# Optimization experiments

Hardware: AMD Instinct MI355X
Metric: run time of the kernel (lower is better)

Reference implementation:

```python
import jax, jax.numpy as jnp
import numpy as np

CUTOFF = 5.0

def ssp(x):
    # shifted softplus: ln(0.5*e^x + 0.5)
    return jax.nn.softplus(x) - jnp.log(2.0).astype(x.dtype)

def cosine_cutoff(r):
    return 0.5 * (jnp.cos(jnp.pi * r / CUTOFF) + 1.0) * (r < CUTOFF).astype(r.dtype)

def setup_inputs() -> dict:
    key = jax.random.key(0)
    ks = jax.random.split(key, 16)
    B, A, N, Nd, F, Din, Dout, Th = 2, 512, 1024, 64, 64, 128, 128, 25
    inp = {}
    inp['x'] = jax.random.normal(ks[0], (B, A, Din), dtype=jnp.float32)
    inp['r_double'] = jax.random.uniform(ks[1], (B, A, Nd), dtype=jnp.float32)
    inp['r_ij'] = jax.random.uniform(ks[2], (B, A, N), dtype=jnp.float32)
    inp['r_ik'] = jax.random.uniform(ks[3], (B, A, N), dtype=jnp.float32)
    inp['r_jk'] = jax.random.uniform(ks[4], (B, A, N), dtype=jnp.float32)
    inp['neighbors'] = jax.random.randint(ks[5], (B, A, Nd), 0, A, dtype=jnp.int32)
    inp['neighbor_mask'] = jnp.ones((B, A, Nd), dtype=jnp.float32)
    inp['neighbors_j'] = jax.random.randint(ks[6], (B, A, N), 0, A, dtype=jnp.int32)
    inp['neighbors_k'] = jax.random.randint(ks[7], (B, A, N), 0, A, dtype=jnp.int32)
    inp['triple_masks'] = jnp.ones((B, A, N), dtype=jnp.float32)
    inp['d_ijk'] = jax.random.uniform(ks[8], (B, A, N, Th), dtype=jnp.float32)
    s = 0.1
    inp['W_in2f'] = s * jax.random.normal(ks[9], (Din, F), dtype=jnp.float32)
    inp['W_t1'] = s * jax.random.normal(ks[10], (Th, F), dtype=jnp.float32)
    inp['b_t1'] = jnp.zeros((F,), dtype=jnp.float32)
    inp['W_t2'] = s * jax.random.normal(ks[11], (F, F), dtype=jnp.float32)
    inp['b_t2'] = jnp.zeros((F,), dtype=jnp.float32)
    inp['W_f2out'] = s * jax.random.normal(ks[12], (F, Dout), dtype=jnp.float32)
    inp['b_f2out'] = jnp.zeros((Dout,), dtype=jnp.float32)
    return inp

def reference(x, r_double, r_ij, r_ik, r_jk, neighbors, neighbor_mask,
              neighbors_j, neighbors_k, triple_masks, d_ijk,
              W_in2f, W_t1, b_t1, W_t2, b_t2, W_f2out, b_f2out):
    # Triple filter: 2-layer MLP on angular basis, modulated by cutoffs
    h = ssp(jnp.einsum('bant,tf->banf', d_ijk, W_t1) + b_t1)
    W_triple = jnp.einsum('banf,fg->bang', h, W_t2) + b_t2
    W_triple = W_triple * cosine_cutoff(r_ij)[..., None] * cosine_cutoff(r_ik)[..., None]

    # in2f: (B, A, F)
    y = jnp.einsum('bad,df->baf', x, W_in2f)
    B, A, N = neighbors_j.shape
    F = y.shape[-1]
    # gather neighbor features along atom axis
    yj = jnp.take_along_axis(y, neighbors_j.reshape(B, A * N, 1), axis=1).reshape(B, A, N, F)
    yk = jnp.take_along_axis(y, neighbors_k.reshape(B, A * N, 1), axis=1).reshape(B, A, N, F)
    w_ij = r_ij[..., None]
    w_ik = r_ik[..., None]
    y = (w_ij * yj + w_ik * yk) / (w_ij + w_ik)
    # filter multiply + masked sum aggregation over triples axis
    y = y * W_triple
    y = jnp.sum(y * triple_masks[..., None], axis=2)
    # f2out with shifted-softplus activation
    out = ssp(jnp.einsum('baf,fo->bao', y, W_f2out) + b_f2out)
    return out
```

## Files before the change

kernel.cpp:

```cpp
#include <hip/hip_runtime.h>
#include <hip/hip_fp16.h>

#define BB 2
#define AA 512
#define NN 1024
#define FF 64
#define DIN 128
#define DOUT 128
#define TH 25
#define ASTRIDE 40
#define HSTRIDE 72
#define NSPLIT 4

typedef _Float16 half8 __attribute__((ext_vector_type(8)));
typedef float floatx4 __attribute__((ext_vector_type(4)));

__device__ __forceinline__ float ssp_f(float x) {
    return __logf(0.5f * __expf(x) + 0.5f);
}

__device__ __forceinline__ float cutcos(float r) {
    float c = 0.5f * (__cosf(r * (3.14159265358979323846f / 5.0f)) + 1.0f);
    return (r < 5.0f) ? c : 0.0f;
}

__device__ __forceinline__ __half2 ssp2(__half2 x) {
    const __half2 hlf = __float2half2_rn(0.5f);
    return h2log(__hfma2(h2exp(x), hlf, hlf));
}

__device__ __forceinline__ __half2 pk2(float a, float b) {
    auto v = __builtin_amdgcn_cvt_pkrtz(a, b);
    __half2 r;
    __builtin_memcpy(&r, &v, sizeof(r));
    return r;
}

#define OFF_Y       0
#define OFF_PARTIAL (OFF_Y + (size_t)BB * AA * FF * 2)
#define OFF_B1      (OFF_PARTIAL + (size_t)NSPLIT * BB * AA * FF * 4)
#define OFF_B2      (OFF_B1 + 4 * 64 * 8 * 2)
#define OFF_BC      (OFF_B2 + 8 * 64 * 8 * 2)

__global__ void in2f_prep_kernel(const float* __restrict__ x,
                                 const float* __restrict__ Wi,
                                 _Float16* __restrict__ y,
                                 const float* __restrict__ W_t1, const float* __restrict__ b_t1,
                                 const float* __restrict__ W_t2, const float* __restrict__ b_t2,
                                 _Float16* __restrict__ B1tab, _Float16* __restrict__ B2tab,
                                 float2* __restrict__ bctab) {
    __shared__ float xs[DIN];
    const int ba = blockIdx.x;
    const int t = threadIdx.x;
    xs[t] = x[ba * DIN + t];
    xs[t + 64] = x[ba * DIN + 64 + t];
    __syncthreads();
    float acc = 0.f;
#pragma unroll 8
    for (int d = 0; d < DIN; ++d) acc += xs[d] * Wi[d * FF + t];
    y[ba * FF + t] = (_Float16)acc;

    if (ba == 0) {
        const int lane = t, quad = t >> 4, l16 = t & 15;
#pragma unroll
        for (int g = 0; g < 4; ++g) {
#pragma unroll
            for (int j = 0; j < 8; ++j) {
                int k = quad * 8 + j;
                B1tab[(g * 64 + lane) * 8 + j] =
                    (k < TH) ? (_Float16)W_t1[k * FF + g * 16 + l16] : (_Float16)0.f;
            }
            bctab[g * 64 + lane] = make_float2(b_t1[g * 16 + l16], b_t2[g * 16 + l16]);
#pragma unroll
            for (int q = 0; q < 2; ++q)
#pragma unroll
                for (int j = 0; j < 8; ++j)
                    B2tab[((g * 2 + q) * 64 + lane) * 8 + j] =
                        (_Float16)W_t2[(q * 32 + quad * 8 + j) * FF + g * 16 + l16];
        }
    }
}

__global__ __launch_bounds__(256) void triple_kernel(
    const int* __restrict__ nbrj, const int* __restrict__ nbrk,
    const float* __restrict__ r_ij, const float* __restrict__ r_ik,
    const float* __restrict__ tmask, const float* __restrict__ d_ijk,
    const _Float16* __restrict__ B1tab, const _Float16* __restrict__ B2tab,
    const float2* __restrict__ bctab,
    const _Float16* __restrict__ y_tab, float* __restrict__ partial) {

    __shared__ __align__(16) _Float16 a_tile[4][16 * ASTRIDE];
    __shared__ __align__(16) _Float16 h_tile[4][16 * HSTRIDE];
    __shared__ float red[4][FF];

    const int blk = blockIdx.x;
    const int ba = blk >> 2;
    const int split = blk & 3;
    const int b = ba >> 9;
    const int tid = threadIdx.x;
    const int w = tid >> 6;
    const int lane = tid & 63;
    const int quad = lane >> 4;
    const int l16 = lane & 15;
    const int rA = lane >> 3;
    const int fc = (lane & 7) * 8;

    const long ban = (long)ba * NN;
    const float* dbase = d_ijk + (long)ba * NN * TH;
    const _Float16* yb = y_tab + (long)b * (AA * FF);

    half8 B1[4];
    half8 B2[4][2];
    __half2 b1h[4], b2h[4];
#pragma unroll
    for (int g = 0; g < 4; ++g) {
        B1[g] = *(const half8*)(B1tab + (g * 64 + lane) * 8);
        B2[g][0] = *(const half8*)(B2tab + ((g * 2 + 0) * 64 + lane) * 8);
        B2[g][1] = *(const half8*)(B2tab + ((g * 2 + 1) * 64 + lane) * 8);
        float2 bc = bctab[g * 64 + lane];
        b1h[g] = __float2half2_rn(bc.x);
        b2h[g] = __float2half2_rn(bc.y);
    }

    for (int idx = lane; idx < 16 * 7; idx += 64) {
        int r = idx / 7, c = 25 + idx % 7;
        a_tile[w][r * ASTRIDE + c] = (_Float16)0.f;
    }

    int lofs2[3][2];
#pragma unroll
    for (int m = 0; m < 3; ++m)
#pragma unroll
        for (int e = 0; e < 2; ++e) {
            int s = m * 128 + lane * 2 + e;
            int r = s / TH, c = s - r * TH;
            lofs2[m][e] = r * ASTRIDE + c;
        }
    const int tofs = 15 * ASTRIDE + 9 + lane;

    float acc[8];
#pragma unroll
    for (int i = 0; i < 8; ++i) acc[i] = 0.f;
    const floatx4 zero4 = {0.f, 0.f, 0.f, 0.f};

    float2 pA[3];
    float pT = 0.f;
    __half2 pwj0, pwk0, pwj1, pwk1;
    int pj0, pk0, pj1, pk1;
    {
        const int n0 = (split * 16 + w) * 16;
        const float* dsrc = dbase + n0 * TH;
#pragma unroll
        for (int m = 0; m < 3; ++m) pA[m] = *(const float2*)(dsrc + m * 128 + lane * 2);
        if (lane < 16) pT = dsrc[384 + lane];
        const long n0a = ban + n0 + rA;
        const long n1a = n0a + 8;
        float rij0 = r_ij[n0a], rij1 = r_ij[n1a];
        float rik0 = r_ik[n0a], rik1 = r_ik[n1a];
        float i0 = cutcos(rij0) * cutcos(rik0) * tmask[n0a] / (rij0 + rik0);
        float i1 = cutcos(rij1) * cutcos(rik1) * tmask[n1a] / (rij1 + rik1);
        pwj0 = __float2half2_rn(rij0 * i0); pwk0 = __float2half2_rn(rik0 * i0);
        pwj1 = __float2half2_rn(rij1 * i1); pwk1 = __float2half2_rn(rik1 * i1);
        pj0 = nbrj[n0a]; pj1 = nbrj[n1a];
        pk0 = nbrk[n0a]; pk1 = nbrk[n1a];
    }

#pragma unroll 1
    for (int it = 0; it < NN / (16 * 4 * NSPLIT); ++it) {
        half8 gj0 = *(const half8*)(yb + pj0 * FF + fc);
        half8 gk0 = *(const half8*)(yb + pk0 * FF + fc);
        half8 gj1 = *(const half8*)(yb + pj1 * FF + fc);
        half8 gk1 = *(const half8*)(yb + pk1 * FF + fc);
        __half2 wj0 = pwj0, wk0 = pwk0, wj1 = pwj1, wk1 = pwk1;

#pragma unroll
        for (int m = 0; m < 3; ++m) {
            a_tile[w][lofs2[m][0]] = (_Float16)pA[m].x;
            a_tile[w][lofs2[m][1]] = (_Float16)pA[m].y;
        }
        if (lane < 16) a_tile[w][tofs] = (_Float16)pT;

        if (it + 1 < NN / (16 * 4 * NSPLIT)) {
            const int n0 = (split * 16 + (it + 1) * 4 + w) * 16;
            const float* dn = dbase + n0 * TH;
#pragma unroll
            for (int m = 0; m < 3; ++m) pA[m] = *(const float2*)(dn + m * 128 + lane * 2);
            if (lane < 16) pT = dn[384 + lane];
            const long n0a = ban + n0 + rA;
            const long n1a = n0a + 8;
            float rij0 = r_ij[n0a], rij1 = r_ij[n1a];
            float rik0 = r_ik[n0a], rik1 = r_ik[n1a];
            float i0 = cutcos(rij0) * cutcos(rik0) * tmask[n0a] / (rij0 + rik0);
            float i1 = cutcos(rij1) * cutcos(rik1) * tmask[n1a] / (rij1 + rik1);
            pwj0 = __float2half2_rn(rij0 * i0); pwk0 = __float2half2_rn(rik0 * i0);
            pwj1 = __float2half2_rn(rij1 * i1); pwk1 = __float2half2_rn(rik1 * i1);
            pj0 = nbrj[n0a]; pj1 = nbrj[n1a];
            pk0 = nbrk[n0a]; pk1 = nbrk[n1a];
        }

        half8 afrag = *(const half8*)&a_tile[w][l16 * ASTRIDE + quad * 8];
#pragma unroll
        for (int g = 0; g < 4; ++g) {
            floatx4 hv = __builtin_amdgcn_mfma_f32_16x16x32_f16(afrag, B1[g], zero4, 0, 0, 0);
#pragma unroll
            for (int p = 0; p < 2; ++p) {
                __half2 hh = ssp2(__hadd2(pk2(hv[2 * p], hv[2 * p + 1]), b1h[g]));
                _Float16 lo, hi;
                __builtin_memcpy(&lo, &hh, 2);
                __builtin_memcpy(&hi, (char*)&hh + 2, 2);
                h_tile[w][(quad * 4 + 2 * p) * HSTRIDE + g * 16 + l16] = lo;
                h_tile[w][(quad * 4 + 2 * p + 1) * HSTRIDE + g * 16 + l16] = hi;
            }
        }

        half8 a2q0 = *(const half8*)&h_tile[w][l16 * HSTRIDE + quad * 8];
        half8 a2q1 = *(const half8*)&h_tile[w][l16 * HSTRIDE + 32 + quad * 8];
#pragma unroll
        for (int g = 0; g < 4; ++g) {
            floatx4 w2 = __builtin_amdgcn_mfma_f32_16x16x32_f16(a2q0, B2[g][0], zero4, 0, 0, 0);
            w2 = __builtin_amdgcn_mfma_f32_16x16x32_f16(a2q1, B2[g][1], w2, 0, 0, 0);
#pragma unroll
            for (int p = 0; p < 2; ++p) {
                __half2 fh = __hadd2(pk2(w2[2 * p], w2[2 * p + 1]), b2h[g]);
                _Float16 lo, hi;
                __builtin_memcpy(&lo, &fh, 2);
                __builtin_memcpy(&hi, (char*)&fh + 2, 2);
                h_tile[w][(quad * 4 + 2 * p) * HSTRIDE + g * 16 + l16] = lo;
                h_tile[w][(quad * 4 + 2 * p + 1) * HSTRIDE + g * 16 + l16] = hi;
            }
        }
        half8 f0 = *(const half8*)&h_tile[w][rA * HSTRIDE + fc];
        half8 f1 = *(const half8*)&h_tile[w][(8 + rA) * HSTRIDE + fc];

        const __half2* gj0p = (const __half2*)&gj0;
        const __half2* gk0p = (const __half2*)&gk0;
        const __half2* gj1p = (const __half2*)&gj1;
        const __half2* gk1p = (const __half2*)&gk1;
        const __half2* f0p = (const __half2*)&f0;
        const __half2* f1p = (const __half2*)&f1;
#pragma unroll
        for (int p = 0; p < 4; ++p) {
            __half2 fv0 = __hfma2(wj0, gj0p[p], __hmul2(wk0, gk0p[p]));
            __half2 fv1 = __hfma2(wj1, gj1p[p], __hmul2(wk1, gk1p[p]));
            __half2 tot = __hfma2(f1p[p], fv1, __hmul2(f0p[p], fv0));
            acc[2 * p]     += __low2float(tot);
            acc[2 * p + 1] += __high2float(tot);
        }
    }

#pragma unroll
    for (int i = 0; i < 8; ++i) {
        acc[i] += __shfl_xor(acc[i], 8, 64);
        acc[i] += __shfl_xor(acc[i], 16, 64);
        acc[i] += __shfl_xor(acc[i], 32, 64);
    }
    if (lane < 8)
#pragma unroll
        for (int i = 0; i < 8; ++i) red[w][lane * 8 + i] = acc[i];
    __syncthreads();

    if (tid < FF)
        partial[(split * (BB * AA) + ba) * FF + tid] =
            red[0][tid] + red[1][tid] + red[2][tid] + red[3][tid];
}

__global__ void out_kernel(const float* __restrict__ partial,
                           const float* __restrict__ Wf,
                           const float* __restrict__ bf,
                           float* __restrict__ out) {
    __shared__ float yag[FF];
    const int ba = blockIdx.x;
    const int t = threadIdx.x;
    if (t < FF) {
        float s = 0.f;
#pragma unroll
        for (int sp = 0; sp < NSPLIT; ++sp)
            s += partial[(sp * (BB * AA) + ba) * FF + t];
        yag[t] = s;
    }
    __syncthreads();
    float a = bf[t];
#pragma unroll 8
    for (int f = 0; f < FF; ++f) a += yag[f] * Wf[f * DOUT + t];
    out[(long)ba * DOUT + t] = ssp_f(a);
}

extern "C" void kernel_launch(void* const* d_in, const int* in_sizes, int n_in,
                              void* d_out, int out_size, void* d_ws, size_t ws_size,
                              hipStream_t stream) {
    const float* x       = (const float*)d_in[0];
    const float* r_ij    = (const float*)d_in[2];
    const float* r_ik    = (const float*)d_in[3];
    const int*   nbrj    = (const int*)d_in[7];
    const int*   nbrk    = (const int*)d_in[8];
    const float* tmask   = (const float*)d_in[9];
    const float* d_ijk   = (const float*)d_in[10];
    const float* W_in2f  = (const float*)d_in[11];
    const float* W_t1    = (const float*)d_in[12];
    const float* b_t1    = (const float*)d_in[13];
    const float* W_t2    = (const float*)d_in[14];
    const float* b_t2    = (const float*)d_in[15];
    const float* W_f2out = (const float*)d_in[16];
    const float* b_f2out = (const float*)d_in[17];
    float* out = (float*)d_out;

    char* ws = (char*)d_ws;
    _Float16* y      = (_Float16*)(ws + OFF_Y);
    float* partial   = (float*)(ws + OFF_PARTIAL);
    _Float16* B1tab  = (_Float16*)(ws + OFF_B1);
    _Float16* B2tab  = (_Float16*)(ws + OFF_B2);
    float2* bctab    = (float2*)(ws + OFF_BC);

    in2f_prep_kernel<<<BB * AA, 64, 0, stream>>>(x, W_in2f, y, W_t1, b_t1,
                                                 W_t2, b_t2, B1tab, B2tab, bctab);
    triple_kernel<<<BB * AA * NSPLIT, 256, 0, stream>>>(nbrj, nbrk, r_ij, r_ik,
                                                        tmask, d_ijk, B1tab, B2tab,
                                                        bctab, y, partial);
    out_kernel<<<BB * AA, 128, 0, stream>>>(partial, W_f2out, b_f2out, out);
}
```

Baseline: 254.7 us.

## Transpose MFMA operands for vectorized LDS stores and preload per-triple weights

Swaps the A and B operands of the MFMA calls so each lane holds four consecutive features of one triple. The hidden and filter tiles can then be written with a single 8-byte LDS store instead of four scalar half stores, and the bias table is re-laid out to match. The per-triple cutoff weights and neighbor indices are now computed once per lane up front and distributed with warp shuffles each iteration, rather than reloaded and recomputed redundantly inside the loop. The cost is extra shuffle instructions in the loop, and all the weight math now happens before the loop starts.

```diff
diff --git a/kernel.cpp b/kernel.cpp
--- a/kernel.cpp
+++ b/kernel.cpp
@@ -13,6 +13,7 @@
 #define NSPLIT 4
 
 typedef _Float16 half8 __attribute__((ext_vector_type(8)));
+typedef _Float16 half4v __attribute__((ext_vector_type(4)));
 typedef float floatx4 __attribute__((ext_vector_type(4)));
 
 __device__ __forceinline__ float ssp_f(float x) {
@@ -36,11 +37,18 @@
     return r;
 }
 
+__device__ __forceinline__ half4v pack4(__half2 lo, __half2 hi) {
+    half4v r;
+    __builtin_memcpy(&r, &lo, 4);
+    __builtin_memcpy(reinterpret_cast<char*>(&r) + 4, &hi, 4);
+    return r;
+}
+
 #define OFF_Y       0
 #define OFF_PARTIAL (OFF_Y + (size_t)BB * AA * FF * 2)
 #define OFF_B1      (OFF_PARTIAL + (size_t)NSPLIT * BB * AA * FF * 4)
 #define OFF_B2      (OFF_B1 + 4 * 64 * 8 * 2)
-#define OFF_BC      (OFF_B2 + 8 * 64 * 8 * 2)
+#define OFF_BP      (OFF_B2 + 8 * 64 * 8 * 2)
 
 __global__ void in2f_prep_kernel(const float* __restrict__ x,
                                  const float* __restrict__ Wi,
@@ -48,7 +56,7 @@
                                  const float* __restrict__ W_t1, const float* __restrict__ b_t1,
                                  const float* __restrict__ W_t2, const float* __restrict__ b_t2,
                                  _Float16* __restrict__ B1tab, _Float16* __restrict__ B2tab,
-                                 float2* __restrict__ bctab) {
+                                 _Float16* __restrict__ BPtab) {
     __shared__ float xs[DIN];
     const int ba = blockIdx.x;
     const int t = threadIdx.x;
@@ -70,7 +78,17 @@
                 B1tab[(g * 64 + lane) * 8 + j] =
                     (k < TH) ? (_Float16)W_t1[k * FF + g * 16 + l16] : (_Float16)0.f;
             }
-            bctab[g * 64 + lane] = make_float2(b_t1[g * 16 + l16], b_t2[g * 16 + l16]);
+#pragma unroll
+            for (int e = 0; e < 2; ++e) {
+                BPtab[((g * 2 + e) * 64 + lane) * 2 + 0] =
+                    (_Float16)b_t1[g * 16 + quad * 4 + 2 * e];
+                BPtab[((g * 2 + e) * 64 + lane) * 2 + 1] =
+                    (_Float16)b_t1[g * 16 + quad * 4 + 2 * e + 1];
+                BPtab[1024 + ((g * 2 + e) * 64 + lane) * 2 + 0] =
+                    (_Float16)b_t2[g * 16 + quad * 4 + 2 * e];
+                BPtab[1024 + ((g * 2 + e) * 64 + lane) * 2 + 1] =
+                    (_Float16)b_t2[g * 16 + quad * 4 + 2 * e + 1];
+            }
 #pragma unroll
             for (int q = 0; q < 2; ++q)
 #pragma unroll
@@ -86,7 +104,7 @@
     const float* __restrict__ r_ij, const float* __restrict__ r_ik,
     const float* __restrict__ tmask, const float* __restrict__ d_ijk,
     const _Float16* __restrict__ B1tab, const _Float16* __restrict__ B2tab,
-    const float2* __restrict__ bctab,
+    const _Float16* __restrict__ BPtab,
     const _Float16* __restrict__ y_tab, float* __restrict__ partial) {
 
     __shared__ __align__(16) _Float16 a_tile[4][16 * ASTRIDE];
@@ -111,16 +129,25 @@
 
     half8 B1[4];
     half8 B2[4][2];
-    __half2 b1h[4], b2h[4];
+    __half2 b1p[4][2], b2p[4][2];
 #pragma unroll
     for (int g = 0; g < 4; ++g) {
         B1[g] = *(const half8*)(B1tab + (g * 64 + lane) * 8);
         B2[g][0] = *(const half8*)(B2tab + ((g * 2 + 0) * 64 + lane) * 8);
         B2[g][1] = *(const half8*)(B2tab + ((g * 2 + 1) * 64 + lane) * 8);
-        float2 bc = bctab[g * 64 + lane];
-        b1h[g] = __float2half2_rn(bc.x);
-        b2h[g] = __float2half2_rn(bc.y);
-    }
+#pragma unroll
+        for (int e = 0; e < 2; ++e) {
+            b1p[g][e] = *(const __half2*)(BPtab + ((g * 2 + e) * 64 + lane) * 2);
+            b2p[g][e] = *(const __half2*)(BPtab + 1024 + ((g * 2 + e) * 64 + lane) * 2);
+        }
+    }
+
+    const int myn = (split * 16 + quad * 4 + w) * 16 + l16;
+    const long myna = ban + myn;
+    const float rijL = r_ij[myna], rikL = r_ik[myna];
+    const float ivL = cutcos(rijL) * cutcos(rikL) * tmask[myna] / (rijL + rikL);
+    const float wjf = rijL * ivL, wkf = rikL * ivL;
+    const int pjL = nbrj[myna], pkL = nbrk[myna];
 
     for (int idx = lane; idx < 16 * 7; idx += 64) {
         int r = idx / 7, c = 25 + idx % 7;
@@ -145,33 +172,24 @@
 
     float2 pA[3];
     float pT = 0.f;
-    __half2 pwj0, pwk0, pwj1, pwk1;
-    int pj0, pk0, pj1, pk1;
     {
         const int n0 = (split * 16 + w) * 16;
         const float* dsrc = dbase + n0 * TH;
 #pragma unroll
         for (int m = 0; m < 3; ++m) pA[m] = *(const float2*)(dsrc + m * 128 + lane * 2);
         if (lane < 16) pT = dsrc[384 + lane];
-        const long n0a = ban + n0 + rA;
-        const long n1a = n0a + 8;
-        float rij0 = r_ij[n0a], rij1 = r_ij[n1a];
-        float rik0 = r_ik[n0a], rik1 = r_ik[n1a];
-        float i0 = cutcos(rij0) * cutcos(rik0) * tmask[n0a] / (rij0 + rik0);
-        float i1 = cutcos(rij1) * cutcos(rik1) * tmask[n1a] / (rij1 + rik1);
-        pwj0 = __float2half2_rn(rij0 * i0); pwk0 = __float2half2_rn(rik0 * i0);
-        pwj1 = __float2half2_rn(rij1 * i1); pwk1 = __float2half2_rn(rik1 * i1);
-        pj0 = nbrj[n0a]; pj1 = nbrj[n1a];
-        pk0 = nbrk[n0a]; pk1 = nbrk[n1a];
     }
 
 #pragma unroll 1
     for (int it = 0; it < NN / (16 * 4 * NSPLIT); ++it) {
+        const int sl0 = it * 16 + rA;
+        const int sl1 = sl0 + 8;
+        const int pj0 = __shfl(pjL, sl0), pk0 = __shfl(pkL, sl0);
+        const int pj1 = __shfl(pjL, sl1), pk1 = __shfl(pkL, sl1);
         half8 gj0 = *(const half8*)(yb + pj0 * FF + fc);
         half8 gk0 = *(const half8*)(yb + pk0 * FF + fc);
         half8 gj1 = *(const half8*)(yb + pj1 * FF + fc);
         half8 gk1 = *(const half8*)(yb + pk1 * FF + fc);
-        __half2 wj0 = pwj0, wk0 = pwk0, wj1 = pwj1, wk1 = pwk1;
 
 #pragma unroll
         for (int m = 0; m < 3; ++m) {
@@ -186,48 +204,31 @@
 #pragma unroll
             for (int m = 0; m < 3; ++m) pA[m] = *(const float2*)(dn + m * 128 + lane * 2);
             if (lane < 16) pT = dn[384 + lane];
-            const long n0a = ban + n0 + rA;
-            const long n1a = n0a + 8;
-            float rij0 = r_ij[n0a], rij1 = r_ij[n1a];
-            float rik0 = r_ik[n0a], rik1 = r_ik[n1a];
-            float i0 = cutcos(rij0) * cutcos(rik0) * tmask[n0a] / (rij0 + rik0);
-            float i1 = cutcos(rij1) * cutcos(rik1) * tmask[n1a] / (rij1 + rik1);
-            pwj0 = __float2half2_rn(rij0 * i0); pwk0 = __float2half2_rn(rik0 * i0);
-            pwj1 = __float2half2_rn(rij1 * i1); pwk1 = __float2half2_rn(rik1 * i1);
-            pj0 = nbrj[n0a]; pj1 = nbrj[n1a];
-            pk0 = nbrk[n0a]; pk1 = nbrk[n1a];
-        }
+        }
+
+        const __half2 wj0 = __float2half2_rn(__shfl(wjf, sl0));
+        const __half2 wk0 = __float2half2_rn(__shfl(wkf, sl0));
+        const __half2 wj1 = __float2half2_rn(__shfl(wjf, sl1));
+        const __half2 wk1 = __float2half2_rn(__shfl(wkf, sl1));
 
         half8 afrag = *(const half8*)&a_tile[w][l16 * ASTRIDE + quad * 8];
 #pragma unroll
         for (int g = 0; g < 4; ++g) {
-            floatx4 hv = __builtin_amdgcn_mfma_f32_16x16x32_f16(afrag, B1[g], zero4, 0, 0, 0);
-#pragma unroll
-            for (int p = 0; p < 2; ++p) {
-                __half2 hh = ssp2(__hadd2(pk2(hv[2 * p], hv[2 * p + 1]), b1h[g]));
-                _Float16 lo, hi;
-                __builtin_memcpy(&lo, &hh, 2);
-                __builtin_memcpy(&hi, (char*)&hh + 2, 2);
-                h_tile[w][(quad * 4 + 2 * p) * HSTRIDE + g * 16 + l16] = lo;
-                h_tile[w][(quad * 4 + 2 * p + 1) * HSTRIDE + g * 16 + l16] = hi;
-            }
+            floatx4 hv = __builtin_amdgcn_mfma_f32_16x16x32_f16(B1[g], afrag, zero4, 0, 0, 0);
+            __half2 h01 = ssp2(__hadd2(pk2(hv[0], hv[1]), b1p[g][0]));
+            __half2 h23 = ssp2(__hadd2(pk2(hv[2], hv[3]), b1p[g][1]));
+            *(half4v*)&h_tile[w][l16 * HSTRIDE + g * 16 + quad * 4] = pack4(h01, h23);
         }
 
         half8 a2q0 = *(const half8*)&h_tile[w][l16 * HSTRIDE + quad * 8];
         half8 a2q1 = *(const half8*)&h_tile[w][l16 * HSTRIDE + 32 + quad * 8];
 #pragma unroll
         for (int g = 0; g < 4; ++g) {
-            floatx4 w2 = __builtin_amdgcn_mfma_f32_16x16x32_f16(a2q0, B2[g][0], zero4, 0, 0, 0);
-            w2 = __builtin_amdgcn_mfma_f32_16x16x32_f16(a2q1, B2[g][1], w2, 0, 0, 0);
-#pragma unroll
-            for (int p = 0; p < 2; ++p) {
-                __half2 fh = __hadd2(pk2(w2[2 * p], w2[2 * p + 1]), b2h[g]);
-                _Float16 lo, hi;
-                __builtin_memcpy(&lo, &fh, 2);
-                __builtin_memcpy(&hi, (char*)&fh + 2, 2);
-                h_tile[w][(quad * 4 + 2 * p) * HSTRIDE + g * 16 + l16] = lo;
-                h_tile[w][(quad * 4 + 2 * p + 1) * HSTRIDE + g * 16 + l16] = hi;
-            }
+            floatx4 w2 = __builtin_amdgcn_mfma_f32_16x16x32_f16(B2[g][0], a2q0, zero4, 0, 0, 0);
+            w2 = __builtin_amdgcn_mfma_f32_16x16x32_f16(B2[g][1], a2q1, w2, 0, 0, 0);
+            __half2 f01 = __hadd2(pk2(w2[0], w2[1]), b2p[g][0]);
+            __half2 f23 = __hadd2(pk2(w2[2], w2[3]), b2p[g][1]);
+            *(half4v*)&h_tile[w][l16 * HSTRIDE + g * 16 + quad * 4] = pack4(f01, f23);
         }
         half8 f0 = *(const half8*)&h_tile[w][rA * HSTRIDE + fc];
         half8 f1 = *(const half8*)&h_tile[w][(8 + rA) * HSTRIDE + fc];
@@ -309,12 +310,12 @@
     float* partial   = (float*)(ws + OFF_PARTIAL);
     _Float16* B1tab  = (_Float16*)(ws + OFF_B1);
     _Float16* B2tab  = (_Float16*)(ws + OFF_B2);
-    float2* bctab    = (float2*)(ws + OFF_BC);
+    _Float16* BPtab  = (_Float16*)(ws + OFF_BP);
 
     in2f_prep_kernel<<<BB * AA, 64, 0, stream>>>(x, W_in2f, y, W_t1, b_t1,
-                                                 W_t2, b_t2, B1tab, B2tab, bctab);
+                                                 W_t2, b_t2, B1tab, B2tab, BPtab);
     triple_kernel<<<BB * AA * NSPLIT, 256, 0, stream>>>(nbrj, nbrk, r_ij, r_ik,
                                                         tmask, d_ijk, B1tab, B2tab,
-                                                        bctab, y, partial);
+                                                        BPtab, y, partial);
     out_kernel<<<BB * AA, 128, 0, stream>>>(partial, W_f2out, b_f2out, out);
 }
```

After: 239.1 us. 6.1% less time.
